# Kernel tuning notes

Measured on AMD Instinct MI355X. Metric: run time of the kernel, lower is better.

The kernel has to match this reference:

```python
import jax, jax.numpy as jnp
import numpy as np

D = 128       # d_model
NHEAD = 4
R = 2         # n_rounds
CF = 32       # fine channels
H0, W0 = 40, 52
HF, WF = 160, 208
TEMP = 0.1
THR = 0.2
WIN = 5
STRIDE = 8


def setup_inputs() -> dict:
    key = jax.random.key(0)
    ks = jax.random.split(key, 24)
    s = 0.05
    f = jnp.float32
    n = lambda k, sh: jax.random.normal(k, sh, f)
    inp = {
        'coarse0': n(ks[0], (1, D, H0, W0)),
        'coarse1': n(ks[1], (1, D, H0, W0)),
        'fine0': n(ks[2], (1, CF, HF, WF)),
        'fine1': n(ks[3], (1, CF, HF, WF)),
        'sa_in_w': n(ks[4], (R, 3 * D, D)) * s,
        'sa_in_b': jnp.zeros((R, 3 * D), f),
        'sa_out_w': n(ks[5], (R, D, D)) * s,
        'sa_out_b': jnp.zeros((R, D), f),
        'ca_in_w': n(ks[6], (R, 3 * D, D)) * s,
        'ca_in_b': jnp.zeros((R, 3 * D), f),
        'ca_out_w': n(ks[7], (R, D, D)) * s,
        'ca_out_b': jnp.zeros((R, D), f),
        'sn_g': jnp.ones((R, D), f), 'sn_b': jnp.zeros((R, D), f),
        'cn_g': jnp.ones((R, D), f), 'cn_b': jnp.zeros((R, D), f),
        'ffn_w1': n(ks[8], (R, 2 * D, D)) * s,
        'ffn_b1': jnp.zeros((R, 2 * D), f),
        'ffn_w2': n(ks[9], (R, D, 2 * D)) * s,
        'ffn_b2': jnp.zeros((R, D), f),
        'fn_g': jnp.ones((R, D), f), 'fn_b': jnp.zeros((R, D), f),
        'proj_w': n(ks[10], (CF, CF)) * s,
        'proj_b': jnp.zeros((CF,), f),
    }
    return inp


def _ln(x, g, b):
    m = x.mean(-1, keepdims=True)
    v = ((x - m) ** 2).mean(-1, keepdims=True)
    return (x - m) * jax.lax.rsqrt(v + 1e-5) * g + b


def _mha(xq, xkv, in_w, in_b, out_w, out_b):
    B, Lq, d = xq.shape
    Lk = xkv.shape[1]
    h, dh = NHEAD, D // NHEAD
    q = (xq @ in_w[:d].T + in_b[:d]).reshape(B, Lq, h, dh)
    k = (xkv @ in_w[d:2 * d].T + in_b[d:2 * d]).reshape(B, Lk, h, dh)
    v = (xkv @ in_w[2 * d:].T + in_b[2 * d:]).reshape(B, Lk, h, dh)
    a = jnp.einsum('bqhd,bkhd->bhqk', q, k) / np.float32(np.sqrt(dh))
    a = jax.nn.softmax(a, axis=-1)
    o = jnp.einsum('bhqk,bkhd->bqhd', a, v).reshape(B, Lq, d)
    return o @ out_w.T + out_b


def _forward(coarse0, coarse1, fine0, fine1, sa_in_w, sa_in_b, sa_out_w, sa_out_b,
             ca_in_w, ca_in_b, ca_out_w, ca_out_b, sn_g, sn_b, cn_g, cn_b,
             ffn_w1, ffn_b1, ffn_w2, ffn_b2, fn_g, fn_b, proj_w, proj_b):
    B, C, H, W = coarse0.shape
    f0 = coarse0.reshape(B, C, H * W).transpose(0, 2, 1)
    f1 = coarse1.reshape(B, C, H * W).transpose(0, 2, 1)
    for i in range(R):
        f0 = _ln(f0 + _mha(f0, f0, sa_in_w[i], sa_in_b[i], sa_out_w[i], sa_out_b[i]), sn_g[i], sn_b[i])
        f1 = _ln(f1 + _mha(f1, f1, sa_in_w[i], sa_in_b[i], sa_out_w[i], sa_out_b[i]), sn_g[i], sn_b[i])
        f0c = _mha(f0, f1, ca_in_w[i], ca_in_b[i], ca_out_w[i], ca_out_b[i])
        f1c = _mha(f1, f0, ca_in_w[i], ca_in_b[i], ca_out_w[i], ca_out_b[i])
        f0 = _ln(f0 + f0c, cn_g[i], cn_b[i])
        f1 = _ln(f1 + f1c, cn_g[i], cn_b[i])
        f0 = _ln(f0 + jax.nn.relu(f0 @ ffn_w1[i].T + ffn_b1[i]) @ ffn_w2[i].T + ffn_b2[i], fn_g[i], fn_b[i])
        f1 = _ln(f1 + jax.nn.relu(f1 @ ffn_w1[i].T + ffn_b1[i]) @ ffn_w2[i].T + ffn_b2[i], fn_g[i], fn_b[i])
    # coarse matching: dual softmax + mutual NN
    f0n = f0 / jnp.maximum(jnp.linalg.norm(f0, axis=-1, keepdims=True), 1e-12)
    f1n = f1 / jnp.maximum(jnp.linalg.norm(f1, axis=-1, keepdims=True), 1e-12)
    S = jnp.einsum('bld,bmd->blm', f0n, f1n) / TEMP
    P = jax.nn.softmax(S, axis=-1) * jax.nn.softmax(S, axis=-2)
    P0 = P[0]
    L0 = H * W
    idx0 = jnp.argmax(P0, axis=-1)
    idx1 = jnp.argmax(P0, axis=0)
    conf = P0.max(axis=-1)
    valid = (idx1[idx0] == jnp.arange(L0)) & (conf > THR)
    ar = jnp.arange(L0)
    mk0 = jnp.stack([ar % W, ar // W], 1).astype(jnp.float32)
    mk1 = jnp.stack([idx0 % W, idx0 // W], 1).astype(jnp.float32)
    # fine refinement (vectorized over all L0 candidate matches)
    f0p = jnp.einsum('oc,chw->ohw', proj_w, fine0[0]) + proj_b[:, None, None]
    f1p = jnp.einsum('oc,chw->ohw', proj_w, fine1[0]) + proj_b[:, None, None]
    half = WIN // 2
    fr = STRIDE // 2
    c0 = (mk0 * fr).astype(jnp.int32)
    c1 = (mk1 * fr).astype(jnp.int32)
    Hf, Wf = f0p.shape[1], f0p.shape[2]
    inb = ((c0[:, 0] - half >= 0) & (c0[:, 0] + half < Wf) & (c0[:, 1] - half >= 0) & (c0[:, 1] + half < Hf)
           & (c1[:, 0] - half >= 0) & (c1[:, 0] + half < Wf) & (c1[:, 1] - half >= 0) & (c1[:, 1] + half < Hf))
    off = jnp.arange(WIN) - half
    cy0 = jnp.clip(c0[:, 1], half, Hf - 1 - half)
    cx0 = jnp.clip(c0[:, 0], half, Wf - 1 - half)
    cy1 = jnp.clip(c1[:, 1], half, Hf - 1 - half)
    cx1 = jnp.clip(c1[:, 0], half, Wf - 1 - half)
    center = f0p[:, cy0, cx0]                              # (C, N)
    y1 = cy1[:, None] + off
    x1 = cx1[:, None] + off
    patch1 = f1p[:, y1[:, :, None], x1[:, None, :]]
    corr = jnp.einsum('cn,cnhw->nhw', center, patch1)
    soft = jax.nn.softmax(corr.reshape(-1, WIN * WIN), axis=-1).reshape(-1, WIN, WIN)
    gx = off.astype(jnp.float32)[None, None, :]
    gy = off.astype(jnp.float32)[None, :, None]
    offx = (soft * gx).sum((1, 2))
    offy = (soft * gy).sum((1, 2))
    scale = np.float32(STRIDE // fr)
    pt0 = mk0 * STRIDE + STRIDE // 2
    base1 = mk1 * STRIDE + STRIDE // 2
    delta = jnp.stack([offx, offy], 1) * scale
    pt1 = base1 + jnp.where(inb[:, None], delta, 0.0)
    return P, valid, conf, pt0, pt1


def reference(coarse0, coarse1, fine0, fine1, sa_in_w, sa_in_b, sa_out_w, sa_out_b,
              ca_in_w, ca_in_b, ca_out_w, ca_out_b, sn_g, sn_b, cn_g, cn_b,
              ffn_w1, ffn_b1, ffn_w2, ffn_b2, fn_g, fn_b, proj_w, proj_b):
    return _forward(coarse0, coarse1, fine0, fine1, sa_in_w, sa_in_b, sa_out_w, sa_out_b,
                    ca_in_w, ca_in_b, ca_out_w, ca_out_b, sn_g, sn_b, cn_g, cn_b,
                    ffn_w1, ffn_b1, ffn_w2, ffn_b2, fn_g, fn_b, proj_w, proj_b)
```

## Files before the change

### kernel.cpp

```cpp
#include <hip/hip_runtime.h>
#include <math.h>

#define LTOK 2080
#define DIM 128
#define NH 4
#define W0C 52
#define HFI 160
#define WFI 208
#define NPIX (HFI*WFI)
#define CFCH 32
#define NSPLIT2 3
#define QBLK 64
#define NQB 33
#define PSTRIDE2 2112

#define DOT4(q,k) ((q).x*(k).x + (q).y*(k).y + (q).z*(k).z + (q).w*(k).w)

__global__ __launch_bounds__(256) void transpose_b_kernel(const float* __restrict__ in0,
                                                          const float* __restrict__ in1,
                                                          float* __restrict__ out0,
                                                          float* __restrict__ out1)
{
    const float* in = blockIdx.z ? in1 : in0;
    float* out = blockIdx.z ? out1 : out0;
    __shared__ float T[32][33];
    int l0 = blockIdx.x * 32, c0 = blockIdx.y * 32;
    int t = threadIdx.x;
    #pragma unroll
    for (int e = 0; e < 4; ++e) {
        int idx = t + e * 256; int i = idx >> 5, j = idx & 31;
        T[i][j] = in[(size_t)(c0 + i) * LTOK + l0 + j];
    }
    __syncthreads();
    #pragma unroll
    for (int e = 0; e < 4; ++e) {
        int idx = t + e * 256; int j2 = idx >> 5, i2 = idx & 31;
        out[(size_t)(l0 + j2) * DIM + c0 + i2] = T[i2][j2];
    }
}

__global__ __launch_bounds__(256) void gemm_nt_b2_kernel(const float* __restrict__ A0,
                                                         const float* __restrict__ A1, int lda,
                                                         const float* __restrict__ B, int ldb,
                                                         float* __restrict__ C0,
                                                         float* __restrict__ C1, int ldc,
                                                         int K,
                                                         const float* __restrict__ bias, int relu)
{
    const float* A = blockIdx.z ? A1 : A0;
    float* C = blockIdx.z ? C1 : C0;
    __shared__ float As[32][33];
    __shared__ float Bs[32][33];
    int tid = threadIdx.x;
    int n0 = blockIdx.x * 32, m0 = blockIdx.y * 32;
    int c = tid & 31, r8 = tid >> 5;
    float acc[4] = {0.f, 0.f, 0.f, 0.f};
    for (int k0 = 0; k0 < K; k0 += 32) {
        #pragma unroll
        for (int e = 0; e < 4; ++e) {
            int l = tid + e * 256;
            int i = l >> 5, k = l & 31;
            As[k][i] = A[(size_t)(m0 + i) * lda + k0 + k];
            Bs[k][i] = B[(size_t)(n0 + i) * ldb + k0 + k];
        }
        __syncthreads();
        #pragma unroll
        for (int k = 0; k < 32; ++k) {
            float bv = Bs[k][c];
            #pragma unroll
            for (int jj = 0; jj < 4; ++jj)
                acc[jj] += As[k][4 * r8 + jj] * bv;
        }
        __syncthreads();
    }
    #pragma unroll
    for (int jj = 0; jj < 4; ++jj) {
        float v = acc[jj];
        if (bias) v += bias[n0 + c];
        if (relu) v = fmaxf(v, 0.f);
        C[(size_t)(m0 + 4 * r8 + jj) * ldc + n0 + c] = v;
    }
}

__global__ __launch_bounds__(256) void gemm_score_kernel(const float* __restrict__ A,
                                                         const float* __restrict__ B,
                                                         float* __restrict__ C,
                                                         float2* __restrict__ prs,
                                                         float2* __restrict__ pcs)
{
    __shared__ float As[32][33];
    __shared__ float Bs[32][33];
    __shared__ float cmS[8][32];
    __shared__ float ceS[8][32];
    int tid = threadIdx.x;
    int n0 = blockIdx.x * 32, m0 = blockIdx.y * 32;
    int c = tid & 31, r8 = tid >> 5;
    float acc[4] = {0.f, 0.f, 0.f, 0.f};
    for (int k0 = 0; k0 < 128; k0 += 32) {
        #pragma unroll
        for (int e = 0; e < 4; ++e) {
            int l = tid + e * 256;
            int i = l >> 5, k = l & 31;
            As[k][i] = A[(size_t)(m0 + i) * 128 + k0 + k];
            Bs[k][i] = B[(size_t)(n0 + i) * 128 + k0 + k];
        }
        __syncthreads();
        #pragma unroll
        for (int k = 0; k < 32; ++k) {
            float bv = Bs[k][c];
            #pragma unroll
            for (int jj = 0; jj < 4; ++jj)
                acc[jj] += As[k][4 * r8 + jj] * bv;
        }
        __syncthreads();
    }
    float v[4];
    #pragma unroll
    for (int jj = 0; jj < 4; ++jj) {
        v[jj] = 10.f * acc[jj];
        C[(size_t)(m0 + 4 * r8 + jj) * LTOK + n0 + c] = v[jj];
    }
    #pragma unroll
    for (int jj = 0; jj < 4; ++jj) {
        float m = v[jj];
        #pragma unroll
        for (int mm = 16; mm >= 1; mm >>= 1) m = fmaxf(m, __shfl_xor(m, mm, 32));
        float e = __expf(v[jj] - m);
        #pragma unroll
        for (int mm = 16; mm >= 1; mm >>= 1) e += __shfl_xor(e, mm, 32);
        if (c == 0) prs[(size_t)blockIdx.x * LTOK + m0 + 4 * r8 + jj] = make_float2(m, e);
    }
    float cmx = fmaxf(fmaxf(v[0], v[1]), fmaxf(v[2], v[3]));
    float cex = __expf(v[0] - cmx) + __expf(v[1] - cmx) + __expf(v[2] - cmx) + __expf(v[3] - cmx);
    cmS[r8][c] = cmx; ceS[r8][c] = cex;
    __syncthreads();
    if (r8 == 0) {
        float M = cmS[0][c], S = ceS[0][c];
        #pragma unroll
        for (int k = 1; k < 8; ++k) {
            float m2 = cmS[k][c], s2 = ceS[k][c];
            if (m2 > M) { S = S * __expf(M - m2) + s2; M = m2; }
            else        { S += s2 * __expf(m2 - M); }
        }
        pcs[(size_t)blockIdx.y * LTOK + n0 + c] = make_float2(M, S);
    }
}

__global__ __launch_bounds__(256) void stats_combine_kernel(const float2* __restrict__ prs,
                                                            const float2* __restrict__ pcs,
                                                            float* __restrict__ rowmax,
                                                            float* __restrict__ rsinv,
                                                            float* __restrict__ colmax,
                                                            float* __restrict__ csinv)
{
    int id = blockIdx.x * 256 + threadIdx.x;
    if (id >= 2 * LTOK) return;
    const float2* p = (id < LTOK) ? (prs + id) : (pcs + (id - LTOK));
    float M = -1e30f;
    for (int i = 0; i < 65; ++i) M = fmaxf(M, p[(size_t)i * LTOK].x);
    float S = 0.f;
    for (int i = 0; i < 65; ++i) {
        float2 f = p[(size_t)i * LTOK];
        S += f.y * __expf(f.x - M);
    }
    if (id < LTOK) { rowmax[id] = M; rsinv[id] = 1.f / S; }
    else           { colmax[id - LTOK] = M; csinv[id - LTOK] = 1.f / S; }
}

__global__ __launch_bounds__(256) void dualp_argmax_kernel(float* __restrict__ S,
                                                           const float* __restrict__ rm,
                                                           const float* __restrict__ rsinv,
                                                           const float* __restrict__ cm,
                                                           const float* __restrict__ csinv,
                                                           float* __restrict__ prv,
                                                           int* __restrict__ pri,
                                                           float* __restrict__ pcv,
                                                           int* __restrict__ pci)
{
    __shared__ float cvS[8][32];
    __shared__ int   ciS[8][32];
    int tid = threadIdx.x;
    int n0 = blockIdx.x * 32, m0 = blockIdx.y * 32;
    int c = tid & 31, r8 = tid >> 5;
    int col = n0 + c;
    float cmv = cm[col], csv = csinv[col];
    float p[4];
    #pragma unroll
    for (int jj = 0; jj < 4; ++jj) {
        int row = m0 + 4 * r8 + jj;
        size_t o = (size_t)row * LTOK + col;
        float s = S[o];
        float pv = __expf(2.f * s - rm[row] - cmv) * (rsinv[row] * csv);
        S[o] = pv;
        p[jj] = pv;
    }
    #pragma unroll
    for (int jj = 0; jj < 4; ++jj) {
        float bv = p[jj]; int bi = col;
        #pragma unroll
        for (int mm = 16; mm >= 1; mm >>= 1) {
            float ov = __shfl_xor(bv, mm, 32);
            int   oi = __shfl_xor(bi, mm, 32);
            if (ov > bv || (ov == bv && oi < bi)) { bv = ov; bi = oi; }
        }
        if (c == 0) {
            prv[(size_t)blockIdx.x * LTOK + m0 + 4 * r8 + jj] = bv;
            pri[(size_t)blockIdx.x * LTOK + m0 + 4 * r8 + jj] = bi;
        }
    }
    float bv = p[0]; int bi = m0 + 4 * r8;
    #pragma unroll
    for (int jj = 1; jj < 4; ++jj)
        if (p[jj] > bv) { bv = p[jj]; bi = m0 + 4 * r8 + jj; }
    cvS[r8][c] = bv; ciS[r8][c] = bi;
    __syncthreads();
    if (r8 == 0) {
        #pragma unroll
        for (int k = 1; k < 8; ++k)
            if (cvS[k][c] > bv) { bv = cvS[k][c]; bi = ciS[k][c]; }
        pcv[(size_t)blockIdx.y * LTOK + col] = bv;
        pci[(size_t)blockIdx.y * LTOK + col] = bi;
    }
}

__global__ __launch_bounds__(256) void argmax_combine_kernel(const float* __restrict__ prv,
                                                             const int* __restrict__ pri,
                                                             const float* __restrict__ pcv,
                                                             const int* __restrict__ pci,
                                                             int* __restrict__ idx0,
                                                             float* __restrict__ conf,
                                                             int* __restrict__ idx1)
{
    int id = blockIdx.x * 256 + threadIdx.x;
    if (id >= 2 * LTOK) return;
    if (id < LTOK) {
        float best = -1e30f; int bi = 0;
        for (int i = 0; i < 65; ++i) {
            float v = prv[(size_t)i * LTOK + id];
            if (v > best) { best = v; bi = pri[(size_t)i * LTOK + id]; }
        }
        idx0[id] = bi; conf[id] = best;
    } else {
        int colI = id - LTOK;
        float best = -1e30f; int bi = 0;
        for (int i = 0; i < 65; ++i) {
            float v = pcv[(size_t)i * LTOK + colI];
            if (v > best) { best = v; bi = pci[(size_t)i * LTOK + colI]; }
        }
        idx1[colI] = bi;
    }
}

__global__ __launch_bounds__(256, 3) void mha_partial2_kernel(const float* __restrict__ qkvA,
                                                              const float* __restrict__ qkvB,
                                                              int cross,
                                                              float* __restrict__ part)
{
    __shared__ float Qs[QBLK][36];
    __shared__ float Ks[64][36];
    __shared__ float Vt[32][68];
    __shared__ float Ps[QBLK][68];
    int tid = threadIdx.x;
    int qb = blockIdx.x, ns = blockIdx.z;
    int img = blockIdx.y >> 2, h = blockIdx.y & 3;
    const float* qsrc  = img ? qkvB : qkvA;
    const float* kvsrc = cross ? (img ? qkvA : qkvB) : qsrc;
    int c4 = tid & 15;
    int rg = tid >> 4;
    const int r0 = rg * 4;
    const float sc = 0.17677669529663687f;

    {
        int r = tid >> 2, d8 = (tid & 3) << 3;
        int qr = qb * QBLK + r; qr = qr < LTOK ? qr : (LTOK - 1);
        const float* src = qsrc + (size_t)qr * 384 + h * 32 + d8;
        *(float4*)(&Qs[r][d8])     = *(const float4*)(src);
        *(float4*)(&Qs[r][d8 + 4]) = *(const float4*)(src + 4);
    }
    float a00=0.f,a01=0.f,a10=0.f,a11=0.f,a20=0.f,a21=0.f,a30=0.f,a31=0.f;
    float l0=0.f,l1=0.f,l2=0.f,l3=0.f;
    __syncthreads();

    const int koff = 128 + h * 32, voff = 256 + h * 32;
    for (int t = ns; t < 33; t += NSPLIT2) {
        int j0 = t * 64;
        {
            int r = tid >> 3, d4 = (tid & 7) << 2;
            int j1 = j0 + r, j2 = j0 + r + 32;
            float4 k1 = *(const float4*)(kvsrc + (size_t)j1 * 384 + koff + d4);
            float4 v1 = *(const float4*)(kvsrc + (size_t)j1 * 384 + voff + d4);
            float4 k2 = make_float4(0.f, 0.f, 0.f, 0.f);
            float4 v2 = make_float4(0.f, 0.f, 0.f, 0.f);
            if (j2 < LTOK) {
                k2 = *(const float4*)(kvsrc + (size_t)j2 * 384 + koff + d4);
                v2 = *(const float4*)(kvsrc + (size_t)j2 * 384 + voff + d4);
            }
            *(float4*)(&Ks[r][d4])      = k1;
            *(float4*)(&Ks[r + 32][d4]) = k2;
            Vt[d4 + 0][r] = v1.x; Vt[d4 + 1][r] = v1.y; Vt[d4 + 2][r] = v1.z; Vt[d4 + 3][r] = v1.w;
            Vt[d4 + 0][r + 32] = v2.x; Vt[d4 + 1][r + 32] = v2.y; Vt[d4 + 2][r + 32] = v2.z; Vt[d4 + 3][r + 32] = v2.w;
        }
        __syncthreads();
        float s00=0.f,s01=0.f,s02=0.f,s03=0.f;
        float s10=0.f,s11=0.f,s12=0.f,s13=0.f;
        float s20=0.f,s21=0.f,s22=0.f,s23=0.f;
        float s30=0.f,s31=0.f,s32=0.f,s33=0.f;
        #pragma unroll
        for (int d4 = 0; d4 < 8; ++d4) {
            const int db = d4 << 2;
            float4 k0 = *(const float4*)(&Ks[c4][db]);
            float4 k1 = *(const float4*)(&Ks[c4 + 16][db]);
            float4 k2 = *(const float4*)(&Ks[c4 + 32][db]);
            float4 k3 = *(const float4*)(&Ks[c4 + 48][db]);
            float4 q0 = *(const float4*)(&Qs[r0 + 0][db]);
            float4 q1 = *(const float4*)(&Qs[r0 + 1][db]);
            float4 q2 = *(const float4*)(&Qs[r0 + 2][db]);
            float4 q3 = *(const float4*)(&Qs[r0 + 3][db]);
            s00 += DOT4(q0,k0); s01 += DOT4(q0,k1); s02 += DOT4(q0,k2); s03 += DOT4(q0,k3);
            s10 += DOT4(q1,k0); s11 += DOT4(q1,k1); s12 += DOT4(q1,k2); s13 += DOT4(q1,k3);
            s20 += DOT4(q2,k0); s21 += DOT4(q2,k1); s22 += DOT4(q2,k2); s23 += DOT4(q2,k3);
            s30 += DOT4(q3,k0); s31 += DOT4(q3,k1); s32 += DOT4(q3,k2); s33 += DOT4(q3,k3);
        }
        bool ok0 = (j0 + c4) < LTOK;
        bool ok1 = (j0 + 16 + c4) < LTOK;
        bool ok2 = (j0 + 32 + c4) < LTOK;
        bool ok3 = (j0 + 48 + c4) < LTOK;
        {
            float p0 = ok0 ? __expf(s00 * sc) : 0.f;
            float p1 = ok1 ? __expf(s01 * sc) : 0.f;
            float p2 = ok2 ? __expf(s02 * sc) : 0.f;
            float p3 = ok3 ? __expf(s03 * sc) : 0.f;
            l0 += p0 + p1 + p2 + p3;
            Ps[r0 + 0][c4] = p0; Ps[r0 + 0][c4 + 16] = p1; Ps[r0 + 0][c4 + 32] = p2; Ps[r0 + 0][c4 + 48] = p3;
        }
        {
            float p0 = ok0 ? __expf(s10 * sc) : 0.f;
            float p1 = ok1 ? __expf(s11 * sc) : 0.f;
            float p2 = ok2 ? __expf(s12 * sc) : 0.f;
            float p3 = ok3 ? __expf(s13 * sc) : 0.f;
            l1 += p0 + p1 + p2 + p3;
            Ps[r0 + 1][c4] = p0; Ps[r0 + 1][c4 + 16] = p1; Ps[r0 + 1][c4 + 32] = p2; Ps[r0 + 1][c4 + 48] = p3;
        }
        {
            float p0 = ok0 ? __expf(s20 * sc) : 0.f;
            float p1 = ok1 ? __expf(s21 * sc) : 0.f;
            float p2 = ok2 ? __expf(s22 * sc) : 0.f;
            float p3 = ok3 ? __expf(s23 * sc) : 0.f;
            l2 += p0 + p1 + p2 + p3;
            Ps[r0 + 2][c4] = p0; Ps[r0 + 2][c4 + 16] = p1; Ps[r0 + 2][c4 + 32] = p2; Ps[r0 + 2][c4 + 48] = p3;
        }
        {
            float p0 = ok0 ? __expf(s30 * sc) : 0.f;
            float p1 = ok1 ? __expf(s31 * sc) : 0.f;
            float p2 = ok2 ? __expf(s32 * sc) : 0.f;
            float p3 = ok3 ? __expf(s33 * sc) : 0.f;
            l3 += p0 + p1 + p2 + p3;
            Ps[r0 + 3][c4] = p0; Ps[r0 + 3][c4 + 16] = p1; Ps[r0 + 3][c4 + 32] = p2; Ps[r0 + 3][c4 + 48] = p3;
        }
        __syncthreads();
        #pragma unroll
        for (int j4 = 0; j4 < 16; ++j4) {
            const int jb = j4 << 2;
            float4 v0 = *(const float4*)(&Vt[c4][jb]);
            float4 v1 = *(const float4*)(&Vt[c4 + 16][jb]);
            float4 pq0 = *(const float4*)(&Ps[r0 + 0][jb]);
            float4 pq1 = *(const float4*)(&Ps[r0 + 1][jb]);
            float4 pq2 = *(const float4*)(&Ps[r0 + 2][jb]);
            float4 pq3 = *(const float4*)(&Ps[r0 + 3][jb]);
            a00 += DOT4(pq0,v0); a01 += DOT4(pq0,v1);
            a10 += DOT4(pq1,v0); a11 += DOT4(pq1,v1);
            a20 += DOT4(pq2,v0); a21 += DOT4(pq2,v1);
            a30 += DOT4(pq3,v0); a31 += DOT4(pq3,v1);
        }
        __syncthreads();
    }
    float* pb = part + (size_t)((((size_t)img * NQB + qb) * NH + h) * NSPLIT2 + ns) * PSTRIDE2;
    pb[(r0 + 0) * 32 + c4]      = a00;
    pb[(r0 + 0) * 32 + c4 + 16] = a01;
    pb[(r0 + 1) * 32 + c4]      = a10;
    pb[(r0 + 1) * 32 + c4 + 16] = a11;
    pb[(r0 + 2) * 32 + c4]      = a20;
    pb[(r0 + 2) * 32 + c4 + 16] = a21;
    pb[(r0 + 3) * 32 + c4]      = a30;
    pb[(r0 + 3) * 32 + c4 + 16] = a31;
    #pragma unroll
    for (int mm = 8; mm >= 1; mm >>= 1) {
        l0 += __shfl_xor(l0, mm, 16);
        l1 += __shfl_xor(l1, mm, 16);
        l2 += __shfl_xor(l2, mm, 16);
        l3 += __shfl_xor(l3, mm, 16);
    }
    if (c4 == 0) {
        pb[2048 + r0 + 0] = l0;
        pb[2048 + r0 + 1] = l1;
        pb[2048 + r0 + 2] = l2;
        pb[2048 + r0 + 3] = l3;
    }
}

__global__ __launch_bounds__(256) void mha_combine2_kernel(const float* __restrict__ part,
                                                           float* __restrict__ out0,
                                                           float* __restrict__ out1)
{
    int tid = threadIdx.x;
    int qb = blockIdx.x;
    int img = blockIdx.y >> 2, h = blockIdx.y & 3;
    float* out = img ? out1 : out0;
    int c = tid & 31, rg8 = tid >> 5;
    const float* pb = part + (size_t)(((size_t)img * NQB + qb) * NH + h) * NSPLIT2 * PSTRIDE2;
    #pragma unroll
    for (int jj = 0; jj < 8; ++jj) {
        int row = rg8 * 8 + jj;
        int qrow = qb * QBLK + row;
        if (qrow >= LTOK) continue;
        float num = 0.f, den = 0.f;
        #pragma unroll
        for (int ns = 0; ns < NSPLIT2; ++ns) {
            num += pb[ns * PSTRIDE2 + row * 32 + c];
            den += pb[ns * PSTRIDE2 + 2048 + row];
        }
        out[(size_t)qrow * DIM + h * 32 + c] = num / den;
    }
}

__global__ __launch_bounds__(256) void addln_b_kernel(float* __restrict__ f0,
                                                      float* __restrict__ f1,
                                                      const float* __restrict__ t0,
                                                      const float* __restrict__ t1,
                                                      const float* __restrict__ g,
                                                      const float* __restrict__ b)
{
    float* f = blockIdx.y ? f1 : f0;
    const float* t = blockIdx.y ? t1 : t0;
    int row = blockIdx.x * 4 + (threadIdx.x >> 6);
    int lane = threadIdx.x & 63;
    size_t base = (size_t)row * DIM;
    float x0 = f[base + lane] + t[base + lane];
    float x1 = f[base + lane + 64] + t[base + lane + 64];
    float s = x0 + x1;
    #pragma unroll
    for (int mm = 32; mm >= 1; mm >>= 1) s += __shfl_xor(s, mm, 64);
    float mean = s * (1.f / 128.f);
    float d0 = x0 - mean, d1 = x1 - mean;
    float v = d0 * d0 + d1 * d1;
    #pragma unroll
    for (int mm = 32; mm >= 1; mm >>= 1) v += __shfl_xor(v, mm, 64);
    float rstd = rsqrtf(v * (1.f / 128.f) + 1e-5f);
    f[base + lane]      = d0 * rstd * g[lane] + b[lane];
    f[base + lane + 64] = d1 * rstd * g[lane + 64] + b[lane + 64];
}

__global__ __launch_bounds__(256) void normrows_b_kernel(const float* __restrict__ i0,
                                                         const float* __restrict__ i1,
                                                         float* __restrict__ o0,
                                                         float* __restrict__ o1)
{
    const float* f = blockIdx.y ? i1 : i0;
    float* o = blockIdx.y ? o1 : o0;
    int row = blockIdx.x * 4 + (threadIdx.x >> 6);
    int lane = threadIdx.x & 63;
    size_t base = (size_t)row * DIM;
    float x0 = f[base + lane], x1 = f[base + lane + 64];
    float v = x0 * x0 + x1 * x1;
    #pragma unroll
    for (int mm = 32; mm >= 1; mm >>= 1) v += __shfl_xor(v, mm, 64);
    float inv = 1.f / fmaxf(sqrtf(v), 1e-12f);
    o[base + lane] = x0 * inv;
    o[base + lane + 64] = x1 * inv;
}

__global__ __launch_bounds__(256) void match_kernel(const int* __restrict__ idx0,
                                                    const int* __restrict__ idx1,
                                                    const float* __restrict__ conf,
                                                    float* __restrict__ out_valid,
                                                    float* __restrict__ out_conf,
                                                    float* __restrict__ out_pt0)
{
    int i = blockIdx.x * 256 + threadIdx.x;
    if (i >= LTOK) return;
    int j = idx0[i];
    bool valid = (idx1[j] == i) && (conf[i] > 0.2f);
    out_valid[i] = valid ? 1.f : 0.f;
    out_conf[i] = conf[i];
    out_pt0[2 * i]     = (float)(i % W0C) * 8.f + 4.f;
    out_pt0[2 * i + 1] = (float)(i / W0C) * 8.f + 4.f;
}

__global__ __launch_bounds__(256) void fine_proj_b_kernel(const float* __restrict__ fin0,
                                                          const float* __restrict__ fin1,
                                                          const float* __restrict__ w,
                                                          const float* __restrict__ b,
                                                          float* __restrict__ fout0,
                                                          float* __restrict__ fout1)
{
    const float* fin = blockIdx.y ? fin1 : fin0;
    float* fout = blockIdx.y ? fout1 : fout0;
    __shared__ float ws_[32][32];
    __shared__ float bs[32];
    int t = threadIdx.x;
    #pragma unroll
    for (int e = 0; e < 4; ++e) { int l = t + e * 256; ws_[l >> 5][l & 31] = w[l]; }
    if (t < 32) bs[t] = b[t];
    __syncthreads();
    int p = blockIdx.x * 256 + t;
    if (p >= NPIX) return;
    float x[32];
    #pragma unroll
    for (int cc = 0; cc < 32; ++cc) x[cc] = fin[(size_t)cc * NPIX + p];
    #pragma unroll
    for (int o = 0; o < 32; ++o) {
        float a = bs[o];
        #pragma unroll
        for (int cc = 0; cc < 32; ++cc) a += ws_[o][cc] * x[cc];
        fout[(size_t)o * NPIX + p] = a;
    }
}

__global__ __launch_bounds__(64) void fine_match_kernel(const int* __restrict__ idx0,
                                                        const float* __restrict__ f0p,
                                                        const float* __restrict__ f1p,
                                                        float* __restrict__ out_pt1)
{
    int i = blockIdx.x;
    int l = threadIdx.x;
    int j = idx0[i];
    int m0x = i % W0C, m0y = i / W0C;
    int m1x = j % W0C, m1y = j / W0C;
    int c0x = m0x * 4, c0y = m0y * 4, c1x = m1x * 4, c1y = m1y * 4;
    bool inb = (c0x - 2 >= 0) && (c0x + 2 < WFI) && (c0y - 2 >= 0) && (c0y + 2 < HFI)
            && (c1x - 2 >= 0) && (c1x + 2 < WFI) && (c1y - 2 >= 0) && (c1y + 2 < HFI);
    int cy0 = min(max(c0y, 2), HFI - 3), cx0 = min(max(c0x, 2), WFI - 3);
    int cy1 = min(max(c1y, 2), HFI - 3), cx1 = min(max(c1x, 2), WFI - 3);
    int dy = l / 5 - 2, dx = l % 5 - 2;
    float corr = -1e30f;
    if (l < 25) {
        float a = 0.f;
        int p0 = cy0 * WFI + cx0;
        int p1 = (cy1 + dy) * WFI + (cx1 + dx);
        #pragma unroll
        for (int cc = 0; cc < 32; ++cc)
            a += f0p[(size_t)cc * NPIX + p0] * f1p[(size_t)cc * NPIX + p1];
        corr = a;
    }
    float mx = corr;
    #pragma unroll
    for (int mm = 32; mm >= 1; mm >>= 1) mx = fmaxf(mx, __shfl_xor(mx, mm, 64));
    float p = (l < 25) ? expf(corr - mx) : 0.f;
    float s = p, sx = p * (float)dx, sy = p * (float)dy;
    #pragma unroll
    for (int mm = 32; mm >= 1; mm >>= 1) {
        s  += __shfl_xor(s, mm, 64);
        sx += __shfl_xor(sx, mm, 64);
        sy += __shfl_xor(sy, mm, 64);
    }
    if (l == 0) {
        float offx = sx / s, offy = sy / s;
        float px = (float)m1x * 8.f + 4.f;
        float py = (float)m1y * 8.f + 4.f;
        if (inb) { px += offx * 2.f; py += offy * 2.f; }
        out_pt1[2 * i]     = px;
        out_pt1[2 * i + 1] = py;
    }
}

extern "C" void kernel_launch(void* const* d_in, const int* in_sizes, int n_in,
                              void* d_out, int out_size, void* d_ws, size_t ws_size,
                              hipStream_t stream) {
    (void)in_sizes; (void)n_in; (void)out_size; (void)ws_size;
    const float* coarse0 = (const float*)d_in[0];
    const float* coarse1 = (const float*)d_in[1];
    const float* fine0   = (const float*)d_in[2];
    const float* fine1   = (const float*)d_in[3];
    const float* sa_in_w  = (const float*)d_in[4];
    const float* sa_in_b  = (const float*)d_in[5];
    const float* sa_out_w = (const float*)d_in[6];
    const float* sa_out_b = (const float*)d_in[7];
    const float* ca_in_w  = (const float*)d_in[8];
    const float* ca_in_b  = (const float*)d_in[9];
    const float* ca_out_w = (const float*)d_in[10];
    const float* ca_out_b = (const float*)d_in[11];
    const float* sn_g = (const float*)d_in[12];
    const float* sn_b = (const float*)d_in[13];
    const float* cn_g = (const float*)d_in[14];
    const float* cn_b = (const float*)d_in[15];
    const float* ffn_w1 = (const float*)d_in[16];
    const float* ffn_b1 = (const float*)d_in[17];
    const float* ffn_w2 = (const float*)d_in[18];
    const float* ffn_b2 = (const float*)d_in[19];
    const float* fn_g = (const float*)d_in[20];
    const float* fn_b = (const float*)d_in[21];
    const float* proj_w = (const float*)d_in[22];
    const float* proj_b = (const float*)d_in[23];

    float* w = (float*)d_ws;
    float* f0   = w; w += (size_t)LTOK * DIM;
    float* f1   = w; w += (size_t)LTOK * DIM;
    float* qkv0 = w; w += (size_t)LTOK * 384;
    float* qkv1 = w; w += (size_t)LTOK * 384;
    float* att0 = w; w += (size_t)LTOK * DIM;
    float* att1 = w; w += (size_t)LTOK * DIM;
    float* tmp0 = w; w += (size_t)LTOK * DIM;
    float* tmp1 = w; w += (size_t)LTOK * DIM;
    float* f0n  = w; w += (size_t)LTOK * DIM;
    float* f1n  = w; w += (size_t)LTOK * DIM;
    float* R1   = w; w += (size_t)2745600;
    float* rowmax = w; w += LTOK;
    float* rsinv  = w; w += LTOK;
    float* colmax = w; w += LTOK;
    float* csinv  = w; w += LTOK;
    float* conf   = w; w += LTOK;
    int* idx0 = (int*)w; w += LTOK;
    int* idx1 = (int*)w; w += LTOK;

    float* part = R1;
    float* hid0 = R1;
    float* hid1 = R1 + (size_t)LTOK * 256;
    float* f0p  = R1;
    float* f1p  = R1 + (size_t)CFCH * NPIX;

    float2* prs = (float2*)qkv0;
    float2* pcs = (float2*)(qkv0 + 2 * 65 * LTOK);
    float*  prv = qkv1;
    int*    pri = (int*)(qkv1 + 65 * LTOK);
    float*  pcv = qkv1 + 2 * 65 * LTOK;
    int*    pci = (int*)(qkv1 + 3 * 65 * LTOK);

    float* Pout = (float*)d_out;
    float* out_valid = Pout + (size_t)LTOK * LTOK;
    float* out_conf  = out_valid + LTOK;
    float* out_pt0   = out_conf + LTOK;
    float* out_pt1   = out_pt0 + 2 * LTOK;

    dim3 b256(256);
    dim3 gMHA(NQB, 8, NSPLIT2);
    dim3 gCMB(NQB, 8);
    dim3 gLN(520, 2);
    transpose_b_kernel<<<dim3(65, 4, 2), b256, 0, stream>>>(coarse0, coarse1, f0, f1);

    for (int i = 0; i < 2; ++i) {
        const float* saw = sa_in_w + (size_t)i * 384 * 128;
        const float* sab = sa_in_b + (size_t)i * 384;
        const float* sow = sa_out_w + (size_t)i * 128 * 128;
        const float* sob = sa_out_b + (size_t)i * 128;
        const float* caw = ca_in_w + (size_t)i * 384 * 128;
        const float* cab = ca_in_b + (size_t)i * 384;
        const float* cow = ca_out_w + (size_t)i * 128 * 128;
        const float* cob = ca_out_b + (size_t)i * 128;
        const float* w1 = ffn_w1 + (size_t)i * 256 * 128;
        const float* b1 = ffn_b1 + (size_t)i * 256;
        const float* w2 = ffn_w2 + (size_t)i * 128 * 256;
        const float* b2 = ffn_b2 + (size_t)i * 128;

        gemm_nt_b2_kernel<<<dim3(12, 65, 2), b256, 0, stream>>>(f0, f1, 128, saw, 128, qkv0, qkv1, 384, 128, sab, 0);
        mha_partial2_kernel<<<gMHA, b256, 0, stream>>>(qkv0, qkv1, 0, part);
        mha_combine2_kernel<<<gCMB, b256, 0, stream>>>(part, att0, att1);
        gemm_nt_b2_kernel<<<dim3(4, 65, 2), b256, 0, stream>>>(att0, att1, 128, sow, 128, tmp0, tmp1, 128, 128, sob, 0);
        addln_b_kernel<<<gLN, b256, 0, stream>>>(f0, f1, tmp0, tmp1, sn_g + (size_t)i * 128, sn_b + (size_t)i * 128);

        gemm_nt_b2_kernel<<<dim3(12, 65, 2), b256, 0, stream>>>(f0, f1, 128, caw, 128, qkv0, qkv1, 384, 128, cab, 0);
        mha_partial2_kernel<<<gMHA, b256, 0, stream>>>(qkv0, qkv1, 1, part);
        mha_combine2_kernel<<<gCMB, b256, 0, stream>>>(part, att0, att1);
        gemm_nt_b2_kernel<<<dim3(4, 65, 2), b256, 0, stream>>>(att0, att1, 128, cow, 128, tmp0, tmp1, 128, 128, cob, 0);
        addln_b_kernel<<<gLN, b256, 0, stream>>>(f0, f1, tmp0, tmp1, cn_g + (size_t)i * 128, cn_b + (size_t)i * 128);

        gemm_nt_b2_kernel<<<dim3(8, 65, 2), b256, 0, stream>>>(f0, f1, 128, w1, 128, hid0, hid1, 256, 128, b1, 1);
        gemm_nt_b2_kernel<<<dim3(4, 65, 2), b256, 0, stream>>>(hid0, hid1, 256, w2, 256, tmp0, tmp1, 128, 256, b2, 0);
        addln_b_kernel<<<gLN, b256, 0, stream>>>(f0, f1, tmp0, tmp1, fn_g + (size_t)i * 128, fn_b + (size_t)i * 128);
    }

    normrows_b_kernel<<<gLN, b256, 0, stream>>>(f0, f1, f0n, f1n);
    gemm_score_kernel<<<dim3(65, 65), b256, 0, stream>>>(f0n, f1n, Pout, prs, pcs);
    stats_combine_kernel<<<17, b256, 0, stream>>>(prs, pcs, rowmax, rsinv, colmax, csinv);
    dualp_argmax_kernel<<<dim3(65, 65), b256, 0, stream>>>(Pout, rowmax, rsinv, colmax, csinv,
                                                           prv, pri, pcv, pci);
    argmax_combine_kernel<<<17, b256, 0, stream>>>(prv, pri, pcv, pci, idx0, conf, idx1);
    match_kernel<<<9, b256, 0, stream>>>(idx0, idx1, conf, out_valid, out_conf, out_pt0);

    fine_proj_b_kernel<<<dim3(130, 2), b256, 0, stream>>>(fine0, fine1, proj_w, proj_b, f0p, f1p);
    fine_match_kernel<<<LTOK, dim3(64), 0, stream>>>(idx0, f0p, f1p, out_pt1);
}
```

Baseline: 926.4 us.

## Use 64x64 register-tiled GEMM with float4 loads and split attention keys more

Replaces the 32x32 transformer projection GEMM with a 64x64 tiled kernel. Each thread now computes a 4x4 output block from float4 shared-memory reads, loads its inputs with vectorized global reads, and clamps rows for the ragged M edge. The attention partial split count goes from 3 to 6, so the partial buffer grows. This targets low arithmetic intensity and poor occupancy of the small GEMMs and the attention kernel, at the cost of fewer GEMM blocks and more combine work.

```diff
diff --git a/kernel.cpp b/kernel.cpp
--- a/kernel.cpp
+++ b/kernel.cpp
@@ -9,7 +9,7 @@
 #define WFI 208
 #define NPIX (HFI*WFI)
 #define CFCH 32
-#define NSPLIT2 3
+#define NSPLIT2 6
 #define QBLK 64
 #define NQB 33
 #define PSTRIDE2 2112
@@ -39,47 +39,73 @@
     }
 }
 
-__global__ __launch_bounds__(256) void gemm_nt_b2_kernel(const float* __restrict__ A0,
-                                                         const float* __restrict__ A1, int lda,
-                                                         const float* __restrict__ B, int ldb,
-                                                         float* __restrict__ C0,
-                                                         float* __restrict__ C1, int ldc,
-                                                         int K,
-                                                         const float* __restrict__ bias, int relu)
+__global__ __launch_bounds__(256) void gemm64_nt_b2_kernel(const float* __restrict__ A0,
+                                                           const float* __restrict__ A1, int lda,
+                                                           const float* __restrict__ B, int ldb,
+                                                           float* __restrict__ C0,
+                                                           float* __restrict__ C1, int ldc,
+                                                           int K,
+                                                           const float* __restrict__ bias, int relu,
+                                                           int M)
 {
     const float* A = blockIdx.z ? A1 : A0;
     float* C = blockIdx.z ? C1 : C0;
-    __shared__ float As[32][33];
-    __shared__ float Bs[32][33];
+    __shared__ float As[32][68];
+    __shared__ float Bs[32][68];
     int tid = threadIdx.x;
-    int n0 = blockIdx.x * 32, m0 = blockIdx.y * 32;
-    int c = tid & 31, r8 = tid >> 5;
-    float acc[4] = {0.f, 0.f, 0.f, 0.f};
+    int n0 = blockIdx.x * 64, m0 = blockIdx.y * 64;
+    int cg = tid & 15, rg = tid >> 4;
+    int r0 = rg * 4, c0 = cg * 4;
+    int srow = tid & 63;
+    int skq  = tid >> 6;
+    float4 acc0 = make_float4(0.f,0.f,0.f,0.f);
+    float4 acc1 = make_float4(0.f,0.f,0.f,0.f);
+    float4 acc2 = make_float4(0.f,0.f,0.f,0.f);
+    float4 acc3 = make_float4(0.f,0.f,0.f,0.f);
+
     for (int k0 = 0; k0 < K; k0 += 32) {
-        #pragma unroll
-        for (int e = 0; e < 4; ++e) {
-            int l = tid + e * 256;
-            int i = l >> 5, k = l & 31;
-            As[k][i] = A[(size_t)(m0 + i) * lda + k0 + k];
-            Bs[k][i] = B[(size_t)(n0 + i) * ldb + k0 + k];
-        }
+        int ar = m0 + srow; ar = ar < M ? ar : M - 1;
+        int br = n0 + srow;
+        const float* ap = A + (size_t)ar * lda + k0 + skq * 8;
+        const float* bp = B + (size_t)br * ldb + k0 + skq * 8;
+        float4 av0 = *(const float4*)(ap);
+        float4 av1 = *(const float4*)(ap + 4);
+        float4 bv0 = *(const float4*)(bp);
+        float4 bv1 = *(const float4*)(bp + 4);
+        int kk = skq * 8;
+        As[kk+0][srow] = av0.x; As[kk+1][srow] = av0.y; As[kk+2][srow] = av0.z; As[kk+3][srow] = av0.w;
+        As[kk+4][srow] = av1.x; As[kk+5][srow] = av1.y; As[kk+6][srow] = av1.z; As[kk+7][srow] = av1.w;
+        Bs[kk+0][srow] = bv0.x; Bs[kk+1][srow] = bv0.y; Bs[kk+2][srow] = bv0.z; Bs[kk+3][srow] = bv0.w;
+        Bs[kk+4][srow] = bv1.x; Bs[kk+5][srow] = bv1.y; Bs[kk+6][srow] = bv1.z; Bs[kk+7][srow] = bv1.w;
         __syncthreads();
         #pragma unroll
         for (int k = 0; k < 32; ++k) {
-            float bv = Bs[k][c];
-            #pragma unroll
-            for (int jj = 0; jj < 4; ++jj)
-                acc[jj] += As[k][4 * r8 + jj] * bv;
+            float4 a = *(const float4*)(&As[k][r0]);
+            float4 b = *(const float4*)(&Bs[k][c0]);
+            acc0.x += a.x*b.x; acc0.y += a.x*b.y; acc0.z += a.x*b.z; acc0.w += a.x*b.w;
+            acc1.x += a.y*b.x; acc1.y += a.y*b.y; acc1.z += a.y*b.z; acc1.w += a.y*b.w;
+            acc2.x += a.z*b.x; acc2.y += a.z*b.y; acc2.z += a.z*b.z; acc2.w += a.z*b.w;
+            acc3.x += a.w*b.x; acc3.y += a.w*b.y; acc3.z += a.w*b.z; acc3.w += a.w*b.w;
         }
         __syncthreads();
     }
-    #pragma unroll
-    for (int jj = 0; jj < 4; ++jj) {
-        float v = acc[jj];
-        if (bias) v += bias[n0 + c];
-        if (relu) v = fmaxf(v, 0.f);
-        C[(size_t)(m0 + 4 * r8 + jj) * ldc + n0 + c] = v;
-    }
+    float4 bv = make_float4(0.f,0.f,0.f,0.f);
+    if (bias) bv = *(const float4*)(bias + n0 + c0);
+    acc0.x += bv.x; acc0.y += bv.y; acc0.z += bv.z; acc0.w += bv.w;
+    acc1.x += bv.x; acc1.y += bv.y; acc1.z += bv.z; acc1.w += bv.w;
+    acc2.x += bv.x; acc2.y += bv.y; acc2.z += bv.z; acc2.w += bv.w;
+    acc3.x += bv.x; acc3.y += bv.y; acc3.z += bv.z; acc3.w += bv.w;
+    if (relu) {
+        acc0.x = fmaxf(acc0.x, 0.f); acc0.y = fmaxf(acc0.y, 0.f); acc0.z = fmaxf(acc0.z, 0.f); acc0.w = fmaxf(acc0.w, 0.f);
+        acc1.x = fmaxf(acc1.x, 0.f); acc1.y = fmaxf(acc1.y, 0.f); acc1.z = fmaxf(acc1.z, 0.f); acc1.w = fmaxf(acc1.w, 0.f);
+        acc2.x = fmaxf(acc2.x, 0.f); acc2.y = fmaxf(acc2.y, 0.f); acc2.z = fmaxf(acc2.z, 0.f); acc2.w = fmaxf(acc2.w, 0.f);
+        acc3.x = fmaxf(acc3.x, 0.f); acc3.y = fmaxf(acc3.y, 0.f); acc3.z = fmaxf(acc3.z, 0.f); acc3.w = fmaxf(acc3.w, 0.f);
+    }
+    int gr = m0 + r0;
+    if (gr + 0 < M) *(float4*)(C + (size_t)(gr + 0) * ldc + n0 + c0) = acc0;
+    if (gr + 1 < M) *(float4*)(C + (size_t)(gr + 1) * ldc + n0 + c0) = acc1;
+    if (gr + 2 < M) *(float4*)(C + (size_t)(gr + 2) * ldc + n0 + c0) = acc2;
+    if (gr + 3 < M) *(float4*)(C + (size_t)(gr + 3) * ldc + n0 + c0) = acc3;
 }
 
 __global__ __launch_bounds__(256) void gemm_score_kernel(const float* __restrict__ A,
@@ -603,7 +629,7 @@
     float* tmp1 = w; w += (size_t)LTOK * DIM;
     float* f0n  = w; w += (size_t)LTOK * DIM;
     float* f1n  = w; w += (size_t)LTOK * DIM;
-    float* R1   = w; w += (size_t)2745600;
+    float* R1   = w; w += (size_t)3345408;
     float* rowmax = w; w += LTOK;
     float* rsinv  = w; w += LTOK;
     float* colmax = w; w += LTOK;
@@ -651,20 +677,20 @@
         const float* w2 = ffn_w2 + (size_t)i * 128 * 256;
         const float* b2 = ffn_b2 + (size_t)i * 128;
 
-        gemm_nt_b2_kernel<<<dim3(12, 65, 2), b256, 0, stream>>>(f0, f1, 128, saw, 128, qkv0, qkv1, 384, 128, sab, 0);
+        gemm64_nt_b2_kernel<<<dim3(6, 33, 2), b256, 0, stream>>>(f0, f1, 128, saw, 128, qkv0, qkv1, 384, 128, sab, 0, LTOK);
         mha_partial2_kernel<<<gMHA, b256, 0, stream>>>(qkv0, qkv1, 0, part);
         mha_combine2_kernel<<<gCMB, b256, 0, stream>>>(part, att0, att1);
-        gemm_nt_b2_kernel<<<dim3(4, 65, 2), b256, 0, stream>>>(att0, att1, 128, sow, 128, tmp0, tmp1, 128, 128, sob, 0);
+        gemm64_nt_b2_kernel<<<dim3(2, 33, 2), b256, 0, stream>>>(att0, att1, 128, sow, 128, tmp0, tmp1, 128, 128, sob, 0, LTOK);
         addln_b_kernel<<<gLN, b256, 0, stream>>>(f0, f1, tmp0, tmp1, sn_g + (size_t)i * 128, sn_b + (size_t)i * 128);
 
-        gemm_nt_b2_kernel<<<dim3(12, 65, 2), b256, 0, stream>>>(f0, f1, 128, caw, 128, qkv0, qkv1, 384, 128, cab, 0);
+        gemm64_nt_b2_kernel<<<dim3(6, 33, 2), b256, 0, stream>>>(f0, f1, 128, caw, 128, qkv0, qkv1, 384, 128, cab, 0, LTOK);
         mha_partial2_kernel<<<gMHA, b256, 0, stream>>>(qkv0, qkv1, 1, part);
         mha_combine2_kernel<<<gCMB, b256, 0, stream>>>(part, att0, att1);
-        gemm_nt_b2_kernel<<<dim3(4, 65, 2), b256, 0, stream>>>(att0, att1, 128, cow, 128, tmp0, tmp1, 128, 128, cob, 0);
+        gemm64_nt_b2_kernel<<<dim3(2, 33, 2), b256, 0, stream>>>(att0, att1, 128, cow, 128, tmp0, tmp1, 128, 128, cob, 0, LTOK);
         addln_b_kernel<<<gLN, b256, 0, stream>>>(f0, f1, tmp0, tmp1, cn_g + (size_t)i * 128, cn_b + (size_t)i * 128);
 
-        gemm_nt_b2_kernel<<<dim3(8, 65, 2), b256, 0, stream>>>(f0, f1, 128, w1, 128, hid0, hid1, 256, 128, b1, 1);
-        gemm_nt_b2_kernel<<<dim3(4, 65, 2), b256, 0, stream>>>(hid0, hid1, 256, w2, 256, tmp0, tmp1, 128, 256, b2, 0);
+        gemm64_nt_b2_kernel<<<dim3(4, 33, 2), b256, 0, stream>>>(f0, f1, 128, w1, 128, hid0, hid1, 256, 128, b1, 1, LTOK);
+        gemm64_nt_b2_kernel<<<dim3(2, 33, 2), b256, 0, stream>>>(hid0, hid1, 256, w2, 256, tmp0, tmp1, 128, 256, b2, 0, LTOK);
         addln_b_kernel<<<gLN, b256, 0, stream>>>(f0, f1, tmp0, tmp1, fn_g + (size_t)i * 128, fn_b + (size_t)i * 128);
     }
 
```

New measurement: 799.0 us. 1.16x faster.
